# Optimization experiments

Hardware: AMD Instinct MI355X
Metric: run time of the kernel (lower is better)

Reference implementation:

```python
import jax, jax.numpy as jnp
import numpy as np

C = 512
HEADS = 8
HEAD_DIM = 64
OUT = 2560
NEG = -1.0e12
EPS = 1e-5


def _layernorm(x, g, b):
    mu = jnp.mean(x, axis=-1, keepdims=True)
    var = jnp.mean(jnp.square(x - mu), axis=-1, keepdims=True)
    return (x - mu) * jax.lax.rsqrt(var + EPS) * g + b


def setup_inputs() -> dict:
    key = jax.random.key(0)
    ks = jax.random.split(key, 16)
    s = 0.02
    return {
        "x": jax.random.normal(ks[0], (8, C, 32, 32), dtype=jnp.float32),
        "conv_w": jax.random.normal(ks[1], (C, C), dtype=jnp.float32) * s,
        "conv_b": jnp.zeros((C,), jnp.float32),
        "ln_g": jnp.ones((C,), jnp.float32),
        "ln_b": jnp.zeros((C,), jnp.float32),
        "qkv_w": jax.random.normal(ks[2], (3 * C, C), dtype=jnp.float32) * s,
        "qkv_b": jnp.zeros((3 * C,), jnp.float32),
        "proj_w": jax.random.normal(ks[3], (C, C), dtype=jnp.float32) * s,
        "proj_b": jnp.zeros((C,), jnp.float32),
        "w1": jax.random.normal(ks[4], (C, C), dtype=jnp.float32) * s,
        "b1": jnp.zeros((C,), jnp.float32),
        "w2": jax.random.normal(ks[5], (C, C), dtype=jnp.float32) * s,
        "b2": jnp.zeros((C,), jnp.float32),
        "fc_w": jax.random.normal(ks[6], (OUT, C), dtype=jnp.float32) * s,
        "fc_b": jnp.zeros((OUT,), jnp.float32),
    }


def reference(x, conv_w, conv_b, ln_g, ln_b, qkv_w, qkv_b, proj_w, proj_b,
              w1, b1, w2, b2, fc_w, fc_b):
    B, Cc, H, W = x.shape
    N = H * W
    mk = jax.random.split(jax.random.key(42), 3)

    # Flat1D: conv1x1 == per-pixel linear, then flatten -> [B, N, C]
    t = jnp.einsum('bchw,oc->bhwo', x, conv_w) + conv_b
    t = t.reshape(B, N, Cc)

    # LayerNorm (shared params)
    t = _layernorm(t, ln_g, ln_b)

    # Attention with random additive mask (p=0.5)
    qkv = t @ qkv_w.T + qkv_b  # [B, N, 3C]
    qkv = qkv.reshape(B, N, 3, HEADS, Cc // HEADS)
    q = jnp.transpose(qkv[:, :, 0], (0, 2, 1, 3))  # [B, H, N, D]
    k = jnp.transpose(qkv[:, :, 1], (0, 2, 1, 3))
    v = jnp.transpose(qkv[:, :, 2], (0, 2, 1, 3))
    scale = HEAD_DIM ** (-0.5)
    attn = jnp.einsum('bhnd,bhmd->bhnm', q, k) * scale
    amask = jax.random.bernoulli(mk[0], 0.5, attn.shape)
    attn = attn + amask.astype(attn.dtype) * NEG
    attn = jax.nn.softmax(attn, axis=-1)
    o = jnp.einsum('bhnm,bhmd->bhnd', attn, v)
    o = jnp.transpose(o, (0, 2, 1, 3)).reshape(B, N, Cc)
    t = o @ proj_w.T + proj_b

    # FeedForward with random additive masks
    h = jax.nn.gelu(t @ w1.T + b1, approximate=False)
    m1 = jax.random.bernoulli(mk[1], 0.3, h.shape)
    h = h + m1.astype(h.dtype) * NEG
    t = h @ w2.T + b2
    m2 = jax.random.bernoulli(mk[2], 0.1, t.shape)
    t = t + m2.astype(t.dtype) * NEG

    # LayerNorm (same params), mean over tokens, final fc
    t = _layernorm(t, ln_g, ln_b)
    t = jnp.mean(t, axis=1)  # [B, C]
    return t @ fc_w.T + fc_b
```

## Files before the change

### kernel.cpp

```cpp
#include <hip/hip_runtime.h>
#include <stdint.h>
#include <math.h>

#define NEGV -1.0e12f
#define QSCALE 0.18033688011112042f

typedef __attribute__((ext_vector_type(8))) short bf16x8;
typedef __attribute__((ext_vector_type(4))) float f32x4;
typedef __attribute__((ext_vector_type(8))) ushort u16x8;

#define ROTL1(v, r) ({ uint32_t _d;                                            \
    asm("v_alignbit_b32 %0, %1, %1, %2" : "=v"(_d) : "v"(v), "n"(32 - (r)));   \
    _d; })

#if defined(__has_builtin)
#if __has_builtin(__builtin_amdgcn_exp2f)
#define EXP2(x) __builtin_amdgcn_exp2f(x)
#endif
#endif
#ifndef EXP2
#define EXP2(x) exp2f(x)
#endif

__host__ static void tf2x32_host(uint32_t k0, uint32_t k1, uint32_t c0, uint32_t c1,
                                 uint32_t* o0, uint32_t* o1) {
    uint32_t ks2 = k0 ^ k1 ^ 0x1BD11BDAu;
    uint32_t x0 = c0 + k0, x1 = c1 + k1;
#define TF_RND(r) x0 += x1; x1 = ((x1 << (r)) | (x1 >> (32 - (r)))); x1 ^= x0;
    TF_RND(13) TF_RND(15) TF_RND(26) TF_RND(6)
    x0 += k1;  x1 += ks2 + 1u;
    TF_RND(17) TF_RND(29) TF_RND(16) TF_RND(24)
    x0 += ks2; x1 += k0 + 2u;
    TF_RND(13) TF_RND(15) TF_RND(26) TF_RND(6)
    x0 += k0;  x1 += k1 + 3u;
    TF_RND(17) TF_RND(29) TF_RND(16) TF_RND(24)
    x0 += k1;  x1 += ks2 + 4u;
    TF_RND(13) TF_RND(15) TF_RND(26) TF_RND(6)
    x0 += ks2; x1 += k0 + 5u;
#undef TF_RND
    *o0 = x0; *o1 = x1;
}

__device__ __forceinline__ uint32_t tf_bits(uint32_t k0, uint32_t k1, uint32_t j) {
    const uint32_t ks2 = k0 ^ k1 ^ 0x1BD11BDAu;
    uint32_t x0 = k0, x1 = j + k1;
#define TFR(r) x0 += x1; x1 = ROTL1(x1, r); x1 ^= x0;
    TFR(13) TFR(15) TFR(26) TFR(6)
    x0 += k1;  x1 += ks2 + 1u;
    TFR(17) TFR(29) TFR(16) TFR(24)
    x0 += ks2; x1 += k0 + 2u;
    TFR(13) TFR(15) TFR(26) TFR(6)
    x0 += k0;  x1 += k1 + 3u;
    TFR(17) TFR(29) TFR(16) TFR(24)
    x0 += k1;  x1 += ks2 + 4u;
    TFR(13) TFR(15) TFR(26) TFR(6)
#undef TFR
    return (x0 + ks2) ^ (x1 + (k0 + 5u));
}

__host__ static uint32_t maskT(float p) {
    double t = ceil((double)p * 8388608.0);
    return ((uint32_t)t) << 9;
}

__device__ __forceinline__ ushort f2bf(float x) {
    uint32_t u = __float_as_uint(x);
    u += 0x7fffu + ((u >> 16) & 1u);
    return (ushort)(u >> 16);
}
__device__ __forceinline__ float bf2f(ushort u) {
    return __uint_as_float(((uint32_t)u) << 16);
}

__global__ __launch_bounds__(256) void prep_k(const float* __restrict__ x,
                                              ushort* __restrict__ xt,
                                              const float* __restrict__ s0,
                                              const float* __restrict__ s1,
                                              const float* __restrict__ s2,
                                              const float* __restrict__ s3,
                                              const float* __restrict__ s4,
                                              ushort* __restrict__ wdst)
{
    __shared__ float tile[64][65];
    const int tid = threadIdx.x;
    if (blockIdx.x < 1024) {
        const int id = blockIdx.x;
        const int n0 = (id & 15) * 64, c0 = ((id >> 4) & 7) * 64, b = id >> 7;
        const float* src = x + ((size_t)b * 512 + c0) * 1024 + n0;
#pragma unroll
        for (int i = 0; i < 4; ++i) {
            const int r = (tid >> 4) + i * 16;
            const int col = (tid & 15) * 4;
            float4 v = *(const float4*)(src + (size_t)r * 1024 + col);
            tile[r][col + 0] = v.x; tile[r][col + 1] = v.y;
            tile[r][col + 2] = v.z; tile[r][col + 3] = v.w;
        }
        __syncthreads();
#pragma unroll
        for (int i = 0; i < 2; ++i) {
            const int nl = (tid >> 3) + i * 32;
            const int cb = (tid & 7) * 8;
            u16x8 o;
#pragma unroll
            for (int j = 0; j < 8; ++j) o[j] = f2bf(tile[cb + j][nl]);
            *(u16x8*)(xt + ((size_t)b * 1024 + n0 + nl) * 512 + c0 + cb) = o;
        }
    } else {
        const size_t i = ((size_t)(blockIdx.x - 1024) * 256 + tid) * 8;
        const float* src; size_t off;
        if (i < 262144)       { src = s0; off = 0; }
        else if (i < 1048576) { src = s1; off = 262144; }
        else if (i < 1310720) { src = s2; off = 1048576; }
        else if (i < 1572864) { src = s3; off = 1310720; }
        else                  { src = s4; off = 1572864; }
        const float* p = src + (i - off);
        float4 a = *(const float4*)p;
        float4 b = *(const float4*)(p + 4);
        u16x8 o;
        o[0] = f2bf(a.x); o[1] = f2bf(a.y); o[2] = f2bf(a.z); o[3] = f2bf(a.w);
        o[4] = f2bf(b.x); o[5] = f2bf(b.y); o[6] = f2bf(b.z); o[7] = f2bf(b.w);
        *(u16x8*)(wdst + i) = o;
    }
}

__global__ __launch_bounds__(256) void convln_k(
    const ushort* __restrict__ A, const ushort* __restrict__ W,
    const float* __restrict__ bias,
    const float* __restrict__ g, const float* __restrict__ bln,
    ushort* __restrict__ outb)
{
    __shared__ ushort cbuf[32][520];
    const int tid = threadIdx.x;
    const int wave = tid >> 6, lane = tid & 63;
    const int lg = lane >> 4, lc = lane & 15;
    const int m0 = blockIdx.x * 32;

    f32x4 acc[2][2][4];
#pragma unroll
    for (int t = 0; t < 2; ++t)
#pragma unroll
        for (int i = 0; i < 2; ++i)
#pragma unroll
            for (int j = 0; j < 4; ++j) acc[t][i][j] = (f32x4){0.f, 0.f, 0.f, 0.f};

    const ushort* Ab = A + (size_t)(m0 + lc) * 512 + lg * 8;
    const ushort* Wb0 = W + (size_t)(wave * 64 + lc) * 512 + lg * 8;
    const ushort* Wb1 = W + (size_t)(256 + wave * 64 + lc) * 512 + lg * 8;

#pragma unroll 4
    for (int k0 = 0; k0 < 512; k0 += 32) {
        bf16x8 aq[2], bw0[4], bw1[4];
        aq[0] = *(const bf16x8*)(Ab + k0);
        aq[1] = *(const bf16x8*)(Ab + 16 * 512 + k0);
#pragma unroll
        for (int j = 0; j < 4; ++j) {
            bw0[j] = *(const bf16x8*)(Wb0 + (size_t)j * 16 * 512 + k0);
            bw1[j] = *(const bf16x8*)(Wb1 + (size_t)j * 16 * 512 + k0);
        }
#pragma unroll
        for (int i = 0; i < 2; ++i)
#pragma unroll
            for (int j = 0; j < 4; ++j) {
                acc[0][i][j] = __builtin_amdgcn_mfma_f32_16x16x32_bf16(aq[i], bw0[j], acc[0][i][j], 0, 0, 0);
                acc[1][i][j] = __builtin_amdgcn_mfma_f32_16x16x32_bf16(aq[i], bw1[j], acc[1][i][j], 0, 0, 0);
            }
    }

#pragma unroll
    for (int t = 0; t < 2; ++t) {
        const int o0 = t * 256 + wave * 64;
#pragma unroll
        for (int j = 0; j < 4; ++j) {
            const float bv = bias[o0 + j * 16 + lc];
#pragma unroll
            for (int i = 0; i < 2; ++i)
#pragma unroll
                for (int r = 0; r < 4; ++r)
                    cbuf[i * 16 + lg * 4 + r][o0 + j * 16 + lc] = f2bf(acc[t][i][j][r] + bv);
        }
    }
    __syncthreads();

    const int c0 = lane * 8;
    float4 g0 = *(const float4*)(g + c0);
    float4 g1 = *(const float4*)(g + c0 + 4);
    float4 b0 = *(const float4*)(bln + c0);
    float4 b1 = *(const float4*)(bln + c0 + 4);
    float gg[8] = {g0.x, g0.y, g0.z, g0.w, g1.x, g1.y, g1.z, g1.w};
    float bv8[8] = {b0.x, b0.y, b0.z, b0.w, b1.x, b1.y, b1.z, b1.w};
#pragma unroll
    for (int tt = 0; tt < 8; ++tt) {
        const int row = wave * 8 + tt;
        u16x8 vv = *(const u16x8*)&cbuf[row][c0];
        float xv[8];
#pragma unroll
        for (int i = 0; i < 8; i++) xv[i] = bf2f(vv[i]);
        float s = 0.f;
#pragma unroll
        for (int i = 0; i < 8; i++) s += xv[i];
#pragma unroll
        for (int sh = 32; sh; sh >>= 1) s += __shfl_xor(s, sh, 64);
        const float mu = s * (1.0f / 512.0f);
        float vs = 0.f;
#pragma unroll
        for (int i = 0; i < 8; i++) { float d = xv[i] - mu; vs += d * d; }
#pragma unroll
        for (int sh = 32; sh; sh >>= 1) vs += __shfl_xor(vs, sh, 64);
        const float inv = 1.0f / sqrtf(vs * (1.0f / 512.0f) + 1e-5f);
        u16x8 o;
#pragma unroll
        for (int i = 0; i < 8; i++) o[i] = f2bf((xv[i] - mu) * inv * gg[i] + bv8[i]);
        *(u16x8*)(outb + (size_t)(m0 + row) * 512 + c0) = o;
    }
}

__global__ __launch_bounds__(256) void qkvvt_k(
    const ushort* __restrict__ A, const ushort* __restrict__ W,
    const float* __restrict__ bias,
    ushort* __restrict__ qb, ushort* __restrict__ kb, ushort* __restrict__ vtb)
{
    __shared__ ushort vtile[64][136];
    const int tid = threadIdx.x;
    const int wave = tid >> 6, lane = tid & 63;
    const int lg = lane >> 4, lc = lane & 15;
    const int m0 = blockIdx.x * 128 + wave * 32;
    const int o0 = blockIdx.y * 64;

    f32x4 acc[2][4];
#pragma unroll
    for (int i = 0; i < 2; ++i)
#pragma unroll
        for (int j = 0; j < 4; ++j) acc[i][j] = (f32x4){0.f, 0.f, 0.f, 0.f};

    const ushort* Ab = A + (size_t)(m0 + lc) * 512 + lg * 8;
    const ushort* Wb = W + (size_t)(o0 + lc) * 512 + lg * 8;

#pragma unroll 4
    for (int k0 = 0; k0 < 512; k0 += 32) {
        bf16x8 aq[2], bw[4];
        aq[0] = *(const bf16x8*)(Ab + k0);
        aq[1] = *(const bf16x8*)(Ab + 16 * 512 + k0);
#pragma unroll
        for (int j = 0; j < 4; ++j) bw[j] = *(const bf16x8*)(Wb + (size_t)j * 16 * 512 + k0);
#pragma unroll
        for (int i = 0; i < 2; ++i)
#pragma unroll
            for (int j = 0; j < 4; ++j)
                acc[i][j] = __builtin_amdgcn_mfma_f32_16x16x32_bf16(aq[i], bw[j], acc[i][j], 0, 0, 0);
    }

    float bvv[4];
#pragma unroll
    for (int j = 0; j < 4; ++j) bvv[j] = bias[o0 + j * 16 + lc];

    if (blockIdx.y < 16) {
#pragma unroll
        for (int i = 0; i < 2; ++i) {
#pragma unroll
            for (int j = 0; j < 4; ++j) {
#pragma unroll
                for (int r = 0; r < 4; ++r) {
                    const int m = m0 + i * 16 + lg * 4 + r;
                    const int o = o0 + j * 16 + lc;
                    float v = acc[i][j][r] + bvv[j];
                    const int s = o >> 9, hh = (o >> 6) & 7, d = o & 63;
                    const int b = m >> 10, n = m & 1023;
                    const int bh = b * 8 + hh;
                    ushort* dst = (s == 0) ? qb : kb;
                    const float scl = (s == 0) ? QSCALE : 1.0f;
                    dst[((size_t)bh * 1024 + n) * 64 + d] = f2bf(v * scl);
                }
            }
        }
    } else {
        const int mloc0 = wave * 32;
#pragma unroll
        for (int i = 0; i < 2; ++i)
#pragma unroll
            for (int j = 0; j < 4; ++j)
#pragma unroll
                for (int r = 0; r < 4; ++r)
                    vtile[j * 16 + lc][mloc0 + i * 16 + lg * 4 + r] = f2bf(acc[i][j][r] + bvv[j]);
        __syncthreads();
        const int hh = blockIdx.y - 16;
        const int mb0 = blockIdx.x * 128;
        const int b = mb0 >> 10, n0 = mb0 & 1023;
        const int bh = b * 8 + hh;
        const int d = tid >> 2, ng = (tid & 3) * 32;
        ushort* dst = vtb + ((size_t)bh * 64 + d) * 1024 + n0 + ng;
#pragma unroll
        for (int q8 = 0; q8 < 4; ++q8) {
            u16x8 o;
#pragma unroll
            for (int e = 0; e < 8; ++e) o[e] = vtile[d][ng + q8 * 8 + e];
            *(u16x8*)(dst + q8 * 8) = o;
        }
    }
}

__global__ __launch_bounds__(256) void attn_k(
    const ushort* __restrict__ qb, const ushort* __restrict__ kb,
    const ushort* __restrict__ vtb, ushort* __restrict__ ob,
    uint32_t km0, uint32_t km1)
{
    __shared__ ushort plds[4][16][40];
    const int tid = threadIdx.x;
    const int wave = tid >> 6, lane = tid & 63;
    const int bh = blockIdx.x & 63;
    const int qt = blockIdx.x >> 6;
    const int b = bh >> 3, h = bh & 7;
    const int q0 = qt * 64 + wave * 16;
    const int lg = lane >> 4, lc = lane & 15;

    const ushort* qp = qb + (size_t)bh * 65536;

    bf16x8 aq0 = *(const bf16x8*)(qp + (size_t)(q0 + lc) * 64 + lg * 8);
    bf16x8 aq1 = *(const bf16x8*)(qp + (size_t)(q0 + lc) * 64 + 32 + lg * 8);

    f32x4 zero = {0.f, 0.f, 0.f, 0.f};
    f32x4 oacc[4] = {zero, zero, zero, zero};
    float D[4] = {0.f, 0.f, 0.f, 0.f};

    uint32_t jr[4];
#pragma unroll
    for (int r = 0; r < 4; ++r)
        jr[r] = ((uint32_t)bh * 1024u + (uint32_t)(q0 + lg * 4 + r)) * 1024u + (uint32_t)lc;

    const ushort* krow = kb + (size_t)bh * 65536 + (size_t)lc * 64 + lg * 8;
    const ushort* vrow = vtb + (size_t)bh * 65536 + (size_t)lc * 1024 + lg * 8;

    for (int ch = 0; ch < 32; ++ch) {
        bf16x8 bk00 = *(const bf16x8*)(krow);
        bf16x8 bk01 = *(const bf16x8*)(krow + 32);
        bf16x8 bk10 = *(const bf16x8*)(krow + 1024);
        bf16x8 bk11 = *(const bf16x8*)(krow + 1056);

        f32x4 s0 = __builtin_amdgcn_mfma_f32_16x16x32_bf16(aq0, bk00, zero, 0, 0, 0);
        s0 = __builtin_amdgcn_mfma_f32_16x16x32_bf16(aq1, bk01, s0, 0, 0, 0);
        f32x4 s1 = __builtin_amdgcn_mfma_f32_16x16x32_bf16(aq0, bk10, zero, 0, 0, 0);
        s1 = __builtin_amdgcn_mfma_f32_16x16x32_bf16(aq1, bk11, s1, 0, 0, 0);

#pragma unroll
        for (int r = 0; r < 4; ++r) {
            const uint32_t bits0 = tf_bits(km0, km1, jr[r]);
            const uint32_t bits1 = tf_bits(km0, km1, jr[r] + 16u);
            jr[r] += 32u;
            const float pv0 = ((int)bits0 < 0) ? EXP2(s0[r]) : 0.f;
            const float pv1 = ((int)bits1 < 0) ? EXP2(s1[r]) : 0.f;
            D[r] += pv0 + pv1;
            uint32_t pk;
            asm("v_cvt_pk_bf16_f32 %0, %1, %2" : "=v"(pk) : "v"(pv0), "v"(pv1));
            plds[wave][lg * 4 + r][lc] = (ushort)pk;
            plds[wave][lg * 4 + r][lc + 16] = (ushort)(pk >> 16);
        }

        bf16x8 pa = *(const bf16x8*)&plds[wave][lc][lg * 8];

#pragma unroll
        for (int dt = 0; dt < 4; ++dt) {
            bf16x8 bv = *(const bf16x8*)(vrow + (size_t)dt * 16384);
            oacc[dt] = __builtin_amdgcn_mfma_f32_16x16x32_bf16(pa, bv, oacc[dt], 0, 0, 0);
        }
        krow += 2048;
        vrow += 32;
    }

#pragma unroll
    for (int r = 0; r < 4; ++r) {
#pragma unroll
        for (int sh = 1; sh < 16; sh <<= 1) D[r] += __shfl_xor(D[r], sh, 64);
    }

#pragma unroll
    for (int r = 0; r < 4; ++r) {
        const int q = q0 + lg * 4 + r;
        const float inv = 1.0f / D[r];
        ushort* orow = ob + ((size_t)b * 1024 + q) * 512 + h * 64;
#pragma unroll
        for (int dt = 0; dt < 4; ++dt) orow[dt * 16 + lc] = f2bf(oacc[dt][r] * inv);
    }
}

__global__ __launch_bounds__(512) void ff_k(
    const ushort* __restrict__ ob,
    const ushort* __restrict__ wproj, const float* __restrict__ pjb,
    const ushort* __restrict__ ww1, const float* __restrict__ b1v,
    const ushort* __restrict__ ww2, const float* __restrict__ b2v,
    const float* __restrict__ g, const float* __restrict__ bln,
    float* __restrict__ pblock,
    uint32_t k10, uint32_t k11, uint32_t k20, uint32_t k21,
    uint32_t T1, uint32_t T2)
{
    __shared__ ushort bufA[16][520];
    __shared__ float stats[16][8][2];
    const int tid = threadIdx.x;
    const int wave = tid >> 6, lane = tid & 63;
    const int lg = lane >> 4, lc = lane & 15;
    const int b = blockIdx.x & 7, tg = blockIdx.x >> 3;

    {
        const int row = tid >> 5, c0 = (tid & 31) * 16;
        const ushort* src = ob + ((size_t)(b * 1024 + tg * 16 + row)) * 512 + c0;
        *(u16x8*)&bufA[row][c0] = *(const u16x8*)src;
        *(u16x8*)&bufA[row][c0 + 8] = *(const u16x8*)(src + 8);
    }
    __syncthreads();

    const int o0 = wave * 64;
    const int mg0 = b * 1024 + tg * 16 + lg * 4;
    f32x4 zero = {0.f, 0.f, 0.f, 0.f};

    f32x4 acc[4] = {zero, zero, zero, zero};
    {
        const ushort* Wb = wproj + (size_t)(o0 + lc) * 512 + lg * 8;
#pragma unroll 4
        for (int k0 = 0; k0 < 512; k0 += 32) {
            bf16x8 a0 = *(const bf16x8*)&bufA[lc][k0 + lg * 8];
#pragma unroll
            for (int j = 0; j < 4; ++j) {
                bf16x8 bw = *(const bf16x8*)(Wb + (size_t)j * 16 * 512 + k0);
                acc[j] = __builtin_amdgcn_mfma_f32_16x16x32_bf16(a0, bw, acc[j], 0, 0, 0);
            }
        }
    }
    float bias4[4];
#pragma unroll
    for (int j = 0; j < 4; ++j) bias4[j] = pjb[o0 + j * 16 + lc];
    __syncthreads();
#pragma unroll
    for (int j = 0; j < 4; ++j)
#pragma unroll
        for (int r = 0; r < 4; ++r)
            bufA[lg * 4 + r][o0 + j * 16 + lc] = f2bf(acc[j][r] + bias4[j]);
    __syncthreads();

#pragma unroll
    for (int j = 0; j < 4; ++j) acc[j] = zero;
    {
        const ushort* Wb = ww1 + (size_t)(o0 + lc) * 512 + lg * 8;
#pragma unroll 4
        for (int k0 = 0; k0 < 512; k0 += 32) {
            bf16x8 a0 = *(const bf16x8*)&bufA[lc][k0 + lg * 8];
#pragma unroll
            for (int j = 0; j < 4; ++j) {
                bf16x8 bw = *(const bf16x8*)(Wb + (size_t)j * 16 * 512 + k0);
                acc[j] = __builtin_amdgcn_mfma_f32_16x16x32_bf16(a0, bw, acc[j], 0, 0, 0);
            }
        }
    }
#pragma unroll
    for (int j = 0; j < 4; ++j) bias4[j] = b1v[o0 + j * 16 + lc];
    __syncthreads();
#pragma unroll
    for (int j = 0; j < 4; ++j) {
#pragma unroll
        for (int r = 0; r < 4; ++r) {
            float v = acc[j][r] + bias4[j];
            v = 0.5f * v * (1.0f + erff(v * 0.70710678118654752f));
            const uint32_t jidx = (uint32_t)((mg0 + r) * 512 + o0 + j * 16 + lc);
            if (tf_bits(k10, k11, jidx) < T1) v += NEGV;
            bufA[lg * 4 + r][o0 + j * 16 + lc] = f2bf(v);
        }
    }
    __syncthreads();

#pragma unroll
    for (int j = 0; j < 4; ++j) acc[j] = zero;
    {
        const ushort* Wb = ww2 + (size_t)(o0 + lc) * 512 + lg * 8;
#pragma unroll 4
        for (int k0 = 0; k0 < 512; k0 += 32) {
            bf16x8 a0 = *(const bf16x8*)&bufA[lc][k0 + lg * 8];
#pragma unroll
            for (int j = 0; j < 4; ++j) {
                bf16x8 bw = *(const bf16x8*)(Wb + (size_t)j * 16 * 512 + k0);
                acc[j] = __builtin_amdgcn_mfma_f32_16x16x32_bf16(a0, bw, acc[j], 0, 0, 0);
            }
        }
    }
#pragma unroll
    for (int j = 0; j < 4; ++j) bias4[j] = b2v[o0 + j * 16 + lc];
    float t2v[4][4];
#pragma unroll
    for (int j = 0; j < 4; ++j) {
#pragma unroll
        for (int r = 0; r < 4; ++r) {
            float v = acc[j][r] + bias4[j];
            const uint32_t jidx = (uint32_t)((mg0 + r) * 512 + o0 + j * 16 + lc);
            if (tf_bits(k20, k21, jidx) < T2) v += NEGV;
            t2v[j][r] = v;
        }
    }

    float rs[4], rq[4];
#pragma unroll
    for (int r = 0; r < 4; ++r) {
        float s = 0.f, q = 0.f;
#pragma unroll
        for (int j = 0; j < 4; ++j) { s += t2v[j][r]; q += t2v[j][r] * t2v[j][r]; }
#pragma unroll
        for (int sh = 1; sh < 16; sh <<= 1) {
            s += __shfl_xor(s, sh, 64);
            q += __shfl_xor(q, sh, 64);
        }
        rs[r] = s; rq[r] = q;
    }
    if (lc == 0) {
#pragma unroll
        for (int r = 0; r < 4; ++r) {
            stats[lg * 4 + r][wave][0] = rs[r];
            stats[lg * 4 + r][wave][1] = rq[r];
        }
    }
    __syncthreads();
    float mu[4], inv[4];
#pragma unroll
    for (int r = 0; r < 4; ++r) {
        float S = 0.f, S2 = 0.f;
#pragma unroll
        for (int w = 0; w < 8; ++w) { S += stats[lg * 4 + r][w][0]; S2 += stats[lg * 4 + r][w][1]; }
        const float m = S * (1.0f / 512.0f);
        const float var = S2 * (1.0f / 512.0f) - m * m;
        mu[r] = m;
        inv[r] = 1.0f / sqrtf(var + 1e-5f);
    }
    float gld[4], bld[4];
#pragma unroll
    for (int j = 0; j < 4; ++j) {
        gld[j] = g[o0 + j * 16 + lc];
        bld[j] = bln[o0 + j * 16 + lc];
    }
    float ps[4] = {0.f, 0.f, 0.f, 0.f};
#pragma unroll
    for (int j = 0; j < 4; ++j) {
#pragma unroll
        for (int r = 0; r < 4; ++r)
            ps[j] += (t2v[j][r] - mu[r]) * inv[r] * gld[j] + bld[j];
    }
#pragma unroll
    for (int j = 0; j < 4; ++j) {
        ps[j] += __shfl_xor(ps[j], 16, 64);
        ps[j] += __shfl_xor(ps[j], 32, 64);
    }
    if (lg == 0) {
#pragma unroll
        for (int j = 0; j < 4; ++j)
            pblock[((size_t)(b * 64 + tg)) * 512 + o0 + j * 16 + lc] = ps[j];
    }
}

__global__ __launch_bounds__(256) void mred2_k(const float* __restrict__ pblock,
                                               float* __restrict__ tm)
{
    const int b = blockIdx.y;
    const int c = blockIdx.x * 256 + threadIdx.x;
    const float* p = pblock + (size_t)b * 64 * 512 + c;
    float s = 0.f;
#pragma unroll 8
    for (int t = 0; t < 64; ++t) s += p[(size_t)t * 512];
    tm[b * 512 + c] = s * (1.0f / 1024.0f);
}

__global__ __launch_bounds__(256) void fc_k(const float* __restrict__ tm,
                                            const float* __restrict__ w,
                                            const float* __restrict__ bias,
                                            float* __restrict__ outp)
{
    const int b = blockIdx.y;
    const int o = blockIdx.x * 256 + threadIdx.x;
    const float* tr = tm + b * 512;
    const float* wr = w + (size_t)o * 512;
    float s = 0.f;
    for (int k = 0; k < 512; k += 4) {
        float4 a = *(const float4*)(tr + k);
        float4 ww = *(const float4*)(wr + k);
        s = fmaf(a.x, ww.x, s); s = fmaf(a.y, ww.y, s);
        s = fmaf(a.z, ww.z, s); s = fmaf(a.w, ww.w, s);
    }
    outp[b * 2560 + o] = s + bias[o];
}

extern "C" void kernel_launch(void* const* d_in, const int* in_sizes, int n_in,
                              void* d_out, int out_size, void* d_ws, size_t ws_size,
                              hipStream_t stream)
{
    const float* x      = (const float*)d_in[0];
    const float* conv_w = (const float*)d_in[1];
    const float* conv_b = (const float*)d_in[2];
    const float* ln_g   = (const float*)d_in[3];
    const float* ln_b   = (const float*)d_in[4];
    const float* qkv_w  = (const float*)d_in[5];
    const float* qkv_b  = (const float*)d_in[6];
    const float* proj_w = (const float*)d_in[7];
    const float* proj_b = (const float*)d_in[8];
    const float* w1     = (const float*)d_in[9];
    const float* b1     = (const float*)d_in[10];
    const float* w2     = (const float*)d_in[11];
    const float* b2     = (const float*)d_in[12];
    const float* fc_w   = (const float*)d_in[13];
    const float* fc_b   = (const float*)d_in[14];
    float* out = (float*)d_out;

    if (ws_size < (size_t)67108864) return;

    uint32_t mk0a, mk0b, mk1a, mk1b, mk2a, mk2b;
    tf2x32_host(0u, 42u, 0u, 0u, &mk0a, &mk0b);
    tf2x32_host(0u, 42u, 0u, 1u, &mk1a, &mk1b);
    tf2x32_host(0u, 42u, 0u, 2u, &mk2a, &mk2b);
    const uint32_t T_m1 = maskT(0.3f);
    const uint32_t T_m2 = maskT(0.1f);

    char* wsb = (char*)d_ws;
    ushort* xt     = (ushort*)wsb;
    ushort* wts    = (ushort*)(wsb + 8388608);
    ushort* qbuf   = (ushort*)(wsb + 12582912);
    ushort* kbuf   = (ushort*)(wsb + 20971520);
    ushort* vtbuf  = (ushort*)(wsb + 29360128);
    ushort* ln1bf  = (ushort*)(wsb + 37748736);
    float*  pblock = (float*)(wsb + 46137344);
    float*  tm     = (float*)(wsb + 47710208);
    ushort* obuf   = xt;

    ushort* wconv = wts;
    ushort* wqkv  = wts + 262144;
    ushort* wproj = wts + 1048576;
    ushort* ww1   = wts + 1310720;
    ushort* ww2   = wts + 1572864;

    dim3 blk(256);
    prep_k<<<dim3(1920), blk, 0, stream>>>(x, xt, conv_w, qkv_w, proj_w, w1, w2, wts);
    convln_k<<<dim3(256), blk, 0, stream>>>(xt, wconv, conv_b, ln_g, ln_b, ln1bf);
    qkvvt_k<<<dim3(64, 24), blk, 0, stream>>>(ln1bf, wqkv, qkv_b, qbuf, kbuf, vtbuf);
    attn_k<<<dim3(1024), blk, 0, stream>>>(qbuf, kbuf, vtbuf, obuf, mk0a, mk0b);
    ff_k<<<dim3(512), dim3(512), 0, stream>>>(obuf, wproj, proj_b, ww1, b1, ww2, b2,
                                              ln_g, ln_b, pblock,
                                              mk1a, mk1b, mk2a, mk2b, T_m1, T_m2);
    mred2_k<<<dim3(2, 8), blk, 0, stream>>>(pblock, tm);
    fc_k<<<dim3(10, 8), blk, 0, stream>>>(tm, fc_w, fc_b, out);
}
```

Before: 350.5 us.

## Retile convln and ff kernels, fuse token-mean reduction into fc

convln_k now runs 512 threads per block, with each wave computing 64 output columns instead of 128. ff_k processes 32 tokens per block instead of 16, so each weight fragment loaded from global memory feeds two MFMA row tiles, halving the weight traffic and the grid size. The separate mean-reduction kernel is folded into the fc kernel, which reduces the 32 partials into shared memory before the dot product. This removes one launch but repeats the reduction in each of the 10 fc column blocks, and the larger ff tile leaves only 256 blocks, which may cut occupancy.

```diff
diff --git a/kernel.cpp b/kernel.cpp
--- a/kernel.cpp
+++ b/kernel.cpp
@@ -123,7 +123,7 @@
     }
 }
 
-__global__ __launch_bounds__(256) void convln_k(
+__global__ __launch_bounds__(512) void convln_k(
     const ushort* __restrict__ A, const ushort* __restrict__ W,
     const float* __restrict__ bias,
     const float* __restrict__ g, const float* __restrict__ bln,
@@ -134,50 +134,39 @@
     const int wave = tid >> 6, lane = tid & 63;
     const int lg = lane >> 4, lc = lane & 15;
     const int m0 = blockIdx.x * 32;
-
-    f32x4 acc[2][2][4];
-#pragma unroll
-    for (int t = 0; t < 2; ++t)
-#pragma unroll
-        for (int i = 0; i < 2; ++i)
-#pragma unroll
-            for (int j = 0; j < 4; ++j) acc[t][i][j] = (f32x4){0.f, 0.f, 0.f, 0.f};
+    const int o0 = wave * 64;
+
+    f32x4 acc[2][4];
+#pragma unroll
+    for (int i = 0; i < 2; ++i)
+#pragma unroll
+        for (int j = 0; j < 4; ++j) acc[i][j] = (f32x4){0.f, 0.f, 0.f, 0.f};
 
     const ushort* Ab = A + (size_t)(m0 + lc) * 512 + lg * 8;
-    const ushort* Wb0 = W + (size_t)(wave * 64 + lc) * 512 + lg * 8;
-    const ushort* Wb1 = W + (size_t)(256 + wave * 64 + lc) * 512 + lg * 8;
+    const ushort* Wb = W + (size_t)(o0 + lc) * 512 + lg * 8;
 
 #pragma unroll 4
     for (int k0 = 0; k0 < 512; k0 += 32) {
-        bf16x8 aq[2], bw0[4], bw1[4];
+        bf16x8 aq[2], bw[4];
         aq[0] = *(const bf16x8*)(Ab + k0);
         aq[1] = *(const bf16x8*)(Ab + 16 * 512 + k0);
 #pragma unroll
-        for (int j = 0; j < 4; ++j) {
-            bw0[j] = *(const bf16x8*)(Wb0 + (size_t)j * 16 * 512 + k0);
-            bw1[j] = *(const bf16x8*)(Wb1 + (size_t)j * 16 * 512 + k0);
-        }
+        for (int j = 0; j < 4; ++j) bw[j] = *(const bf16x8*)(Wb + (size_t)j * 16 * 512 + k0);
 #pragma unroll
         for (int i = 0; i < 2; ++i)
 #pragma unroll
-            for (int j = 0; j < 4; ++j) {
-                acc[0][i][j] = __builtin_amdgcn_mfma_f32_16x16x32_bf16(aq[i], bw0[j], acc[0][i][j], 0, 0, 0);
-                acc[1][i][j] = __builtin_amdgcn_mfma_f32_16x16x32_bf16(aq[i], bw1[j], acc[1][i][j], 0, 0, 0);
-            }
-    }
-
-#pragma unroll
-    for (int t = 0; t < 2; ++t) {
-        const int o0 = t * 256 + wave * 64;
-#pragma unroll
-        for (int j = 0; j < 4; ++j) {
-            const float bv = bias[o0 + j * 16 + lc];
-#pragma unroll
-            for (int i = 0; i < 2; ++i)
-#pragma unroll
-                for (int r = 0; r < 4; ++r)
-                    cbuf[i * 16 + lg * 4 + r][o0 + j * 16 + lc] = f2bf(acc[t][i][j][r] + bv);
-        }
+            for (int j = 0; j < 4; ++j)
+                acc[i][j] = __builtin_amdgcn_mfma_f32_16x16x32_bf16(aq[i], bw[j], acc[i][j], 0, 0, 0);
+    }
+
+#pragma unroll
+    for (int j = 0; j < 4; ++j) {
+        const float bv = bias[o0 + j * 16 + lc];
+#pragma unroll
+        for (int i = 0; i < 2; ++i)
+#pragma unroll
+            for (int r = 0; r < 4; ++r)
+                cbuf[i * 16 + lg * 4 + r][o0 + j * 16 + lc] = f2bf(acc[i][j][r] + bv);
     }
     __syncthreads();
 
@@ -189,8 +178,8 @@
     float gg[8] = {g0.x, g0.y, g0.z, g0.w, g1.x, g1.y, g1.z, g1.w};
     float bv8[8] = {b0.x, b0.y, b0.z, b0.w, b1.x, b1.y, b1.z, b1.w};
 #pragma unroll
-    for (int tt = 0; tt < 8; ++tt) {
-        const int row = wave * 8 + tt;
+    for (int tt = 0; tt < 4; ++tt) {
+        const int row = wave * 4 + tt;
         u16x8 vv = *(const u16x8*)&cbuf[row][c0];
         float xv[8];
 #pragma unroll
@@ -391,35 +380,42 @@
     uint32_t k10, uint32_t k11, uint32_t k20, uint32_t k21,
     uint32_t T1, uint32_t T2)
 {
-    __shared__ ushort bufA[16][520];
-    __shared__ float stats[16][8][2];
+    __shared__ ushort bufA[32][520];
+    __shared__ float stats[32][8][2];
     const int tid = threadIdx.x;
     const int wave = tid >> 6, lane = tid & 63;
     const int lg = lane >> 4, lc = lane & 15;
     const int b = blockIdx.x & 7, tg = blockIdx.x >> 3;
 
     {
-        const int row = tid >> 5, c0 = (tid & 31) * 16;
-        const ushort* src = ob + ((size_t)(b * 1024 + tg * 16 + row)) * 512 + c0;
-        *(u16x8*)&bufA[row][c0] = *(const u16x8*)src;
-        *(u16x8*)&bufA[row][c0 + 8] = *(const u16x8*)(src + 8);
+        const int row = tid >> 4, c0 = (tid & 15) * 32;
+        const ushort* src = ob + ((size_t)(b * 1024 + tg * 32 + row)) * 512 + c0;
+#pragma unroll
+        for (int q8 = 0; q8 < 4; ++q8)
+            *(u16x8*)&bufA[row][c0 + q8 * 8] = *(const u16x8*)(src + q8 * 8);
     }
     __syncthreads();
 
     const int o0 = wave * 64;
-    const int mg0 = b * 1024 + tg * 16 + lg * 4;
+    const int mg0 = b * 1024 + tg * 32;
     f32x4 zero = {0.f, 0.f, 0.f, 0.f};
 
-    f32x4 acc[4] = {zero, zero, zero, zero};
+    f32x4 acc[2][4];
+#pragma unroll
+    for (int i = 0; i < 2; ++i)
+#pragma unroll
+        for (int j = 0; j < 4; ++j) acc[i][j] = zero;
     {
         const ushort* Wb = wproj + (size_t)(o0 + lc) * 512 + lg * 8;
 #pragma unroll 4
         for (int k0 = 0; k0 < 512; k0 += 32) {
             bf16x8 a0 = *(const bf16x8*)&bufA[lc][k0 + lg * 8];
+            bf16x8 a1 = *(const bf16x8*)&bufA[16 + lc][k0 + lg * 8];
 #pragma unroll
             for (int j = 0; j < 4; ++j) {
                 bf16x8 bw = *(const bf16x8*)(Wb + (size_t)j * 16 * 512 + k0);
-                acc[j] = __builtin_amdgcn_mfma_f32_16x16x32_bf16(a0, bw, acc[j], 0, 0, 0);
+                acc[0][j] = __builtin_amdgcn_mfma_f32_16x16x32_bf16(a0, bw, acc[0][j], 0, 0, 0);
+                acc[1][j] = __builtin_amdgcn_mfma_f32_16x16x32_bf16(a1, bw, acc[1][j], 0, 0, 0);
             }
         }
     }
@@ -428,23 +424,29 @@
     for (int j = 0; j < 4; ++j) bias4[j] = pjb[o0 + j * 16 + lc];
     __syncthreads();
 #pragma unroll
-    for (int j = 0; j < 4; ++j)
-#pragma unroll
-        for (int r = 0; r < 4; ++r)
-            bufA[lg * 4 + r][o0 + j * 16 + lc] = f2bf(acc[j][r] + bias4[j]);
-    __syncthreads();
-
-#pragma unroll
-    for (int j = 0; j < 4; ++j) acc[j] = zero;
+    for (int i = 0; i < 2; ++i)
+#pragma unroll
+        for (int j = 0; j < 4; ++j)
+#pragma unroll
+            for (int r = 0; r < 4; ++r)
+                bufA[i * 16 + lg * 4 + r][o0 + j * 16 + lc] = f2bf(acc[i][j][r] + bias4[j]);
+    __syncthreads();
+
+#pragma unroll
+    for (int i = 0; i < 2; ++i)
+#pragma unroll
+        for (int j = 0; j < 4; ++j) acc[i][j] = zero;
     {
         const ushort* Wb = ww1 + (size_t)(o0 + lc) * 512 + lg * 8;
 #pragma unroll 4
         for (int k0 = 0; k0 < 512; k0 += 32) {
             bf16x8 a0 = *(const bf16x8*)&bufA[lc][k0 + lg * 8];
+            bf16x8 a1 = *(const bf16x8*)&bufA[16 + lc][k0 + lg * 8];
 #pragma unroll
             for (int j = 0; j < 4; ++j) {
                 bf16x8 bw = *(const bf16x8*)(Wb + (size_t)j * 16 * 512 + k0);
-                acc[j] = __builtin_amdgcn_mfma_f32_16x16x32_bf16(a0, bw, acc[j], 0, 0, 0);
+                acc[0][j] = __builtin_amdgcn_mfma_f32_16x16x32_bf16(a0, bw, acc[0][j], 0, 0, 0);
+                acc[1][j] = __builtin_amdgcn_mfma_f32_16x16x32_bf16(a1, bw, acc[1][j], 0, 0, 0);
             }
         }
     }
@@ -452,77 +454,93 @@
     for (int j = 0; j < 4; ++j) bias4[j] = b1v[o0 + j * 16 + lc];
     __syncthreads();
 #pragma unroll
-    for (int j = 0; j < 4; ++j) {
-#pragma unroll
-        for (int r = 0; r < 4; ++r) {
-            float v = acc[j][r] + bias4[j];
-            v = 0.5f * v * (1.0f + erff(v * 0.70710678118654752f));
-            const uint32_t jidx = (uint32_t)((mg0 + r) * 512 + o0 + j * 16 + lc);
-            if (tf_bits(k10, k11, jidx) < T1) v += NEGV;
-            bufA[lg * 4 + r][o0 + j * 16 + lc] = f2bf(v);
-        }
-    }
-    __syncthreads();
-
-#pragma unroll
-    for (int j = 0; j < 4; ++j) acc[j] = zero;
+    for (int i = 0; i < 2; ++i) {
+#pragma unroll
+        for (int j = 0; j < 4; ++j) {
+#pragma unroll
+            for (int r = 0; r < 4; ++r) {
+                float v = acc[i][j][r] + bias4[j];
+                v = 0.5f * v * (1.0f + erff(v * 0.70710678118654752f));
+                const uint32_t jidx =
+                    (uint32_t)((mg0 + i * 16 + lg * 4 + r) * 512 + o0 + j * 16 + lc);
+                if (tf_bits(k10, k11, jidx) < T1) v += NEGV;
+                bufA[i * 16 + lg * 4 + r][o0 + j * 16 + lc] = f2bf(v);
+            }
+        }
+    }
+    __syncthreads();
+
+#pragma unroll
+    for (int i = 0; i < 2; ++i)
+#pragma unroll
+        for (int j = 0; j < 4; ++j) acc[i][j] = zero;
     {
         const ushort* Wb = ww2 + (size_t)(o0 + lc) * 512 + lg * 8;
 #pragma unroll 4
         for (int k0 = 0; k0 < 512; k0 += 32) {
             bf16x8 a0 = *(const bf16x8*)&bufA[lc][k0 + lg * 8];
+            bf16x8 a1 = *(const bf16x8*)&bufA[16 + lc][k0 + lg * 8];
 #pragma unroll
             for (int j = 0; j < 4; ++j) {
                 bf16x8 bw = *(const bf16x8*)(Wb + (size_t)j * 16 * 512 + k0);
-                acc[j] = __builtin_amdgcn_mfma_f32_16x16x32_bf16(a0, bw, acc[j], 0, 0, 0);
+                acc[0][j] = __builtin_amdgcn_mfma_f32_16x16x32_bf16(a0, bw, acc[0][j], 0, 0, 0);
+                acc[1][j] = __builtin_amdgcn_mfma_f32_16x16x32_bf16(a1, bw, acc[1][j], 0, 0, 0);
             }
         }
     }
 #pragma unroll
     for (int j = 0; j < 4; ++j) bias4[j] = b2v[o0 + j * 16 + lc];
-    float t2v[4][4];
-#pragma unroll
-    for (int j = 0; j < 4; ++j) {
+    float t2v[2][4][4];
+#pragma unroll
+    for (int i = 0; i < 2; ++i) {
+#pragma unroll
+        for (int j = 0; j < 4; ++j) {
+#pragma unroll
+            for (int r = 0; r < 4; ++r) {
+                float v = acc[i][j][r] + bias4[j];
+                const uint32_t jidx =
+                    (uint32_t)((mg0 + i * 16 + lg * 4 + r) * 512 + o0 + j * 16 + lc);
+                if (tf_bits(k20, k21, jidx) < T2) v += NEGV;
+                t2v[i][j][r] = v;
+            }
+        }
+    }
+
+#pragma unroll
+    for (int i = 0; i < 2; ++i) {
 #pragma unroll
         for (int r = 0; r < 4; ++r) {
-            float v = acc[j][r] + bias4[j];
-            const uint32_t jidx = (uint32_t)((mg0 + r) * 512 + o0 + j * 16 + lc);
-            if (tf_bits(k20, k21, jidx) < T2) v += NEGV;
-            t2v[j][r] = v;
-        }
-    }
-
-    float rs[4], rq[4];
-#pragma unroll
-    for (int r = 0; r < 4; ++r) {
-        float s = 0.f, q = 0.f;
-#pragma unroll
-        for (int j = 0; j < 4; ++j) { s += t2v[j][r]; q += t2v[j][r] * t2v[j][r]; }
-#pragma unroll
-        for (int sh = 1; sh < 16; sh <<= 1) {
-            s += __shfl_xor(s, sh, 64);
-            q += __shfl_xor(q, sh, 64);
-        }
-        rs[r] = s; rq[r] = q;
-    }
-    if (lc == 0) {
+            float s = 0.f, q = 0.f;
+#pragma unroll
+            for (int j = 0; j < 4; ++j) { s += t2v[i][j][r]; q += t2v[i][j][r] * t2v[i][j][r]; }
+#pragma unroll
+            for (int sh = 1; sh < 16; sh <<= 1) {
+                s += __shfl_xor(s, sh, 64);
+                q += __shfl_xor(q, sh, 64);
+            }
+            if (lc == 0) {
+                stats[i * 16 + lg * 4 + r][wave][0] = s;
+                stats[i * 16 + lg * 4 + r][wave][1] = q;
+            }
+        }
+    }
+    __syncthreads();
+    float mu[2][4], inv[2][4];
+#pragma unroll
+    for (int i = 0; i < 2; ++i) {
 #pragma unroll
         for (int r = 0; r < 4; ++r) {
-            stats[lg * 4 + r][wave][0] = rs[r];
-            stats[lg * 4 + r][wave][1] = rq[r];
-        }
-    }
-    __syncthreads();
-    float mu[4], inv[4];
-#pragma unroll
-    for (int r = 0; r < 4; ++r) {
-        float S = 0.f, S2 = 0.f;
-#pragma unroll
-        for (int w = 0; w < 8; ++w) { S += stats[lg * 4 + r][w][0]; S2 += stats[lg * 4 + r][w][1]; }
-        const float m = S * (1.0f / 512.0f);
-        const float var = S2 * (1.0f / 512.0f) - m * m;
-        mu[r] = m;
-        inv[r] = 1.0f / sqrtf(var + 1e-5f);
+            float S = 0.f, S2 = 0.f;
+#pragma unroll
+            for (int w = 0; w < 8; ++w) {
+                S += stats[i * 16 + lg * 4 + r][w][0];
+                S2 += stats[i * 16 + lg * 4 + r][w][1];
+            }
+            const float m = S * (1.0f / 512.0f);
+            const float var = S2 * (1.0f / 512.0f) - m * m;
+            mu[i][r] = m;
+            inv[i][r] = 1.0f / sqrtf(var + 1e-5f);
+        }
     }
     float gld[4], bld[4];
 #pragma unroll
@@ -532,11 +550,12 @@
     }
     float ps[4] = {0.f, 0.f, 0.f, 0.f};
 #pragma unroll
-    for (int j = 0; j < 4; ++j) {
-#pragma unroll
-        for (int r = 0; r < 4; ++r)
-            ps[j] += (t2v[j][r] - mu[r]) * inv[r] * gld[j] + bld[j];
-    }
+    for (int i = 0; i < 2; ++i)
+#pragma unroll
+        for (int j = 0; j < 4; ++j)
+#pragma unroll
+            for (int r = 0; r < 4; ++r)
+                ps[j] += (t2v[i][j][r] - mu[i][r]) * inv[i][r] * gld[j] + bld[j];
 #pragma unroll
     for (int j = 0; j < 4; ++j) {
         ps[j] += __shfl_xor(ps[j], 16, 64);
@@ -545,34 +564,33 @@
     if (lg == 0) {
 #pragma unroll
         for (int j = 0; j < 4; ++j)
-            pblock[((size_t)(b * 64 + tg)) * 512 + o0 + j * 16 + lc] = ps[j];
-    }
-}
-
-__global__ __launch_bounds__(256) void mred2_k(const float* __restrict__ pblock,
-                                               float* __restrict__ tm)
+            pblock[((size_t)(b * 32 + tg)) * 512 + o0 + j * 16 + lc] = ps[j];
+    }
+}
+
+__global__ __launch_bounds__(256) void fc2_k(const float* __restrict__ pblock,
+                                             const float* __restrict__ w,
+                                             const float* __restrict__ bias,
+                                             float* __restrict__ outp)
 {
+    __shared__ float tmld[512];
     const int b = blockIdx.y;
-    const int c = blockIdx.x * 256 + threadIdx.x;
-    const float* p = pblock + (size_t)b * 64 * 512 + c;
-    float s = 0.f;
+    const int tid = threadIdx.x;
+#pragma unroll
+    for (int cc = 0; cc < 2; ++cc) {
+        const int c = tid + cc * 256;
+        const float* p = pblock + (size_t)(b * 32) * 512 + c;
+        float s = 0.f;
 #pragma unroll 8
-    for (int t = 0; t < 64; ++t) s += p[(size_t)t * 512];
-    tm[b * 512 + c] = s * (1.0f / 1024.0f);
-}
-
-__global__ __launch_bounds__(256) void fc_k(const float* __restrict__ tm,
-                                            const float* __restrict__ w,
-                                            const float* __restrict__ bias,
-                                            float* __restrict__ outp)
-{
-    const int b = blockIdx.y;
-    const int o = blockIdx.x * 256 + threadIdx.x;
-    const float* tr = tm + b * 512;
+        for (int t = 0; t < 32; ++t) s += p[(size_t)t * 512];
+        tmld[c] = s * (1.0f / 1024.0f);
+    }
+    __syncthreads();
+    const int o = blockIdx.x * 256 + tid;
     const float* wr = w + (size_t)o * 512;
     float s = 0.f;
     for (int k = 0; k < 512; k += 4) {
-        float4 a = *(const float4*)(tr + k);
+        float4 a = *(const float4*)(tmld + k);
         float4 ww = *(const float4*)(wr + k);
         s = fmaf(a.x, ww.x, s); s = fmaf(a.y, ww.y, s);
         s = fmaf(a.z, ww.z, s); s = fmaf(a.w, ww.w, s);
@@ -618,7 +636,6 @@
     ushort* vtbuf  = (ushort*)(wsb + 29360128);
     ushort* ln1bf  = (ushort*)(wsb + 37748736);
     float*  pblock = (float*)(wsb + 46137344);
-    float*  tm     = (float*)(wsb + 47710208);
     ushort* obuf   = xt;
 
     ushort* wconv = wts;
@@ -629,12 +646,11 @@
 
     dim3 blk(256);
     prep_k<<<dim3(1920), blk, 0, stream>>>(x, xt, conv_w, qkv_w, proj_w, w1, w2, wts);
-    convln_k<<<dim3(256), blk, 0, stream>>>(xt, wconv, conv_b, ln_g, ln_b, ln1bf);
+    convln_k<<<dim3(256), dim3(512), 0, stream>>>(xt, wconv, conv_b, ln_g, ln_b, ln1bf);
     qkvvt_k<<<dim3(64, 24), blk, 0, stream>>>(ln1bf, wqkv, qkv_b, qbuf, kbuf, vtbuf);
     attn_k<<<dim3(1024), blk, 0, stream>>>(qbuf, kbuf, vtbuf, obuf, mk0a, mk0b);
-    ff_k<<<dim3(512), dim3(512), 0, stream>>>(obuf, wproj, proj_b, ww1, b1, ww2, b2,
+    ff_k<<<dim3(256), dim3(512), 0, stream>>>(obuf, wproj, proj_b, ww1, b1, ww2, b2,
                                               ln_g, ln_b, pblock,
                                               mk1a, mk1b, mk2a, mk2b, T_m1, T_m2);
-    mred2_k<<<dim3(2, 8), blk, 0, stream>>>(pblock, tm);
-    fc_k<<<dim3(10, 8), blk, 0, stream>>>(tm, fc_w, fc_b, out);
-}
+    fc2_k<<<dim3(10, 8), blk, 0, stream>>>(pblock, fc_w, fc_b, out);
+}
```

Measured after the change: 323.0 us. 7.9% less time.
